# Optimization experiments

Measured on AMD Instinct MI355X. Metric: run time of the kernel, lower is better.

The kernel has to match this reference:

```python
import jax, jax.numpy as jnp
import numpy as np

N_HEAD = 16
ROPE_CACHE = 2500  # Rotary module caches tables of length 2500
NEG_INF = -1e30


def _rope_tables(head_dim):
    inv_freq = 1.0 / (10000.0 ** (jnp.arange(0, head_dim, 2, dtype=jnp.float32) / head_dim))
    t = jnp.arange(ROPE_CACHE, dtype=jnp.float32)
    freqs = t[:, None] * inv_freq[None, :]            # (2500, head_dim//2)
    emb = jnp.concatenate([freqs, freqs], axis=-1)    # (2500, head_dim)
    return jnp.cos(emb), jnp.sin(emb)


def _rotate_half(x):
    h = x.shape[-1] // 2
    return jnp.concatenate([-x[..., h:], x[..., :h]], axis=-1)


def setup_inputs() -> dict:
    key = jax.random.key(0)
    ks = jax.random.split(key, 8)
    B, S, D = 2, 2048, 1024
    H = N_HEAD
    hd = D // H
    return {
        "qx": jax.random.normal(ks[0], (B, S, D), jnp.float32),
        "kvx": jax.random.normal(ks[1], (B, S, D), jnp.float32),
        "k_cache": jnp.zeros((B, H, S, hd), jnp.float32),
        "v_cache": jnp.zeros((B, H, S, hd), jnp.float32),
        "Wq": jax.random.normal(ks[2], (D, D), jnp.float32) * 0.02,
        "bq": jnp.zeros((D,), jnp.float32),
        "Wk": jax.random.normal(ks[3], (D, D), jnp.float32) * 0.02,
        "Wv": jax.random.normal(ks[4], (D, D), jnp.float32) * 0.02,
        "bv": jnp.zeros((D,), jnp.float32),
        "Wo": jax.random.normal(ks[5], (D, D), jnp.float32) * 0.02,
        "bo": jnp.zeros((D,), jnp.float32),
        "q_positions": jnp.arange(S, dtype=jnp.int32),
        "kv_positions": jnp.arange(S, dtype=jnp.int32),
    }


def reference(qx, kvx, k_cache, v_cache, Wq, bq, Wk, Wv, bv, Wo, bo, q_positions, kv_positions):
    B, Sq, D = qx.shape
    H = N_HEAD
    hd = D // H
    Skv = kvx.shape[1]
    cos, sin = _rope_tables(hd)
    # sqrt_qk_scale = sqrt(1) = 1, folded out.

    def rope(x, pos):  # x: (B, S, H, hd)
        c = cos[pos][None, :, None, :]
        s = sin[pos][None, :, None, :]
        return x * c + _rotate_half(x) * s

    # projections (torch Linear: y = x @ W.T + b; key has no bias)
    q = (qx @ Wq.T + bq).reshape(B, Sq, H, hd)
    q = rope(q, q_positions).transpose(0, 2, 1, 3)            # (B,H,Sq,hd)
    k = (kvx @ Wk.T).reshape(B, Skv, H, hd)
    k = rope(k, kv_positions).transpose(0, 2, 1, 3)           # (B,H,Skv,hd)
    v = (kvx @ Wv.T + bv).reshape(B, Skv, H, hd).transpose(0, 2, 1, 3)

    # KV-cache scatter update: k_cache[:, :, kv_positions] = k
    k_cache = k_cache.at[:, :, kv_positions].set(k)
    v_cache = v_cache.at[:, :, kv_positions].set(v)
    Sc = k_cache.shape[2]

    # SDPA (causal), scaled by 1/sqrt(head_dim) as in F.scaled_dot_product_attention
    scores = jnp.einsum('bhqd,bhkd->bhqk', q, k_cache) / jnp.sqrt(jnp.float32(hd))
    causal = jnp.arange(Sq)[:, None] >= jnp.arange(Sc)[None, :]
    scores = jnp.where(causal[None, None], scores, NEG_INF)
    attn = jax.nn.softmax(scores, axis=-1)
    wv = jnp.einsum('bhqk,bhkd->bhqd', attn, v_cache)

    out = wv.transpose(0, 2, 1, 3).reshape(B, Sq, D) @ Wo.T + bo
    return out
```

## Files before the change

### kernel.cpp

```cpp
#include <hip/hip_runtime.h>
#include <cstdint>
#include <cstddef>

#define NH   16
#define SEQ  2048
#define DM   1024
#define HD   64
#define KDIM 1024
#define MROWS 4096
#define CH   2

using short8  = __attribute__((ext_vector_type(8))) short;
using short4v = __attribute__((ext_vector_type(4))) short;
using floatx4 = __attribute__((ext_vector_type(4))) float;

__device__ __forceinline__ short f2bf(float f) {
  unsigned int u = __float_as_uint(f);
  u += 0x7fffu + ((u >> 16) & 1u);
  return (short)(u >> 16);
}
__device__ __forceinline__ float bf2f(short s) {
  return __uint_as_float(((unsigned int)(unsigned short)s) << 16);
}
__device__ __forceinline__ unsigned int pktrunc(float lo, float hi) {
  return __builtin_amdgcn_perm(__float_as_uint(hi), __float_as_uint(lo),
                               0x07060302u);
}

__device__ __forceinline__ void async_ld16(const void* g, void* l) {
  __builtin_amdgcn_global_load_lds(
      (const __attribute__((address_space(1))) void*)g,
      (__attribute__((address_space(3))) void*)l, 16, 0, 0);
}

struct Cvt8 {
  const float* src[8];
  void* dst[8];
  int n[8];
  const int* pos[8];
};

__global__ void convert8(Cvt8 a) {
  const int which = blockIdx.y;
  const int stride = gridDim.x * blockDim.x;
  if (which < 6) {
    const float4* s = (const float4*)a.src[which];
    short4v* d = (short4v*)a.dst[which];
    const int n4 = a.n[which] >> 2;
    for (int i = blockIdx.x * blockDim.x + threadIdx.x; i < n4; i += stride) {
      float4 v = s[i];
      short4v o;
      o.x = f2bf(v.x); o.y = f2bf(v.y); o.z = f2bf(v.z); o.w = f2bf(v.w);
      d[i] = o;
    }
  } else {
    const int* pos = a.pos[which];
    float2* d = (float2*)a.dst[which];
    const int n = a.n[which];
    for (int i = blockIdx.x * blockDim.x + threadIdx.x; i < n; i += stride) {
      int s = i >> 5, d1 = i & 31;
      float fr = __powf(10000.f, -(float)d1 * (1.f / 32.f));
      float ang = (float)pos[s] * fr;
      float sn, cs;
      __sincosf(ang, &sn, &cs);
      d[i] = make_float2(cs, sn);
    }
  }
}

__device__ __forceinline__ void gemm_core(const short* __restrict__ A,
                                          const short* __restrict__ B,
                                          int row0, int col0,
                                          short* As, short* Bs,
                                          floatx4 (&acc)[4][4], int tid) {
  const int lane = tid & 63;
  const int w = tid >> 6;
  const int quad = lane >> 4;
  const int ln = lane & 15;
  const int wr = w >> 1, wc = w & 1;
  const int swz = (quad ^ ((ln >> 1) & 3)) * 8;

#pragma unroll
  for (int i = 0; i < 4; ++i)
#pragma unroll
    for (int j = 0; j < 4; ++j) acc[i][j] = (floatx4){0.f, 0.f, 0.f, 0.f};

  for (int k0 = 0; k0 < KDIM; k0 += 64) {
    __syncthreads();
#pragma unroll
    for (int g = 0; g < 4; ++g) {
      int slot = g * 256 + tid;
      int kk = slot >> 9;
      int row = (slot >> 2) & 127;
      int grp = (slot & 3) ^ ((slot >> 3) & 3);
      int src = k0 + kk * 32 + grp * 8;
      async_ld16(A + (size_t)(row0 + row) * KDIM + src, As + slot * 8);
      async_ld16(B + (size_t)(col0 + row) * KDIM + src, Bs + slot * 8);
    }
    __syncthreads();

#pragma unroll
    for (int ks = 0; ks < 2; ++ks) {
      short8 af[4], bfr[4];
#pragma unroll
      for (int i = 0; i < 4; ++i)
        af[i] = *(const short8*)(As + ks * 4096 + (wr * 64 + i * 16 + ln) * 32 + swz);
#pragma unroll
      for (int j = 0; j < 4; ++j)
        bfr[j] = *(const short8*)(Bs + ks * 4096 + (wc * 64 + j * 16 + ln) * 32 + swz);
#pragma unroll
      for (int i = 0; i < 4; ++i)
#pragma unroll
        for (int j = 0; j < 4; ++j)
          acc[i][j] = __builtin_amdgcn_mfma_f32_16x16x32_bf16(af[i], bfr[j], acc[i][j], 0, 0, 0);
    }
  }
}

__global__ __launch_bounds__(256) void proj_gemm(
    const short* __restrict__ qxb, const short* __restrict__ kvxb,
    const short* __restrict__ Wqb, const short* __restrict__ Wkb,
    const short* __restrict__ Wvb,
    const float* __restrict__ bq, const float* __restrict__ bv,
    short* __restrict__ Qo, short* __restrict__ Ko, short* __restrict__ Vt,
    const float2* __restrict__ qtab, const float2* __restrict__ ktab) {
  __shared__ __align__(16) short As[128 * 64];
  __shared__ __align__(16) short Bs[128 * 64];

  const int tid = threadIdx.x;
  const int lane = tid & 63;
  const int w = tid >> 6;
  const int quad = lane >> 4;
  const int ln = lane & 15;
  const int wr = w >> 1, wc = w & 1;
  const int z = blockIdx.z;

  int row0, col0;
  const short *A, *B;
  if (z == 2) {
    A = Wvb; B = kvxb;
    row0 = blockIdx.x * 128;
    col0 = blockIdx.y * 128;
  } else {
    A = z ? kvxb : qxb;
    B = z ? Wkb : Wqb;
    row0 = blockIdx.y * 128;
    col0 = blockIdx.x * 128;
  }

  floatx4 acc[4][4];
  gemm_core(A, B, row0, col0, As, Bs, acc, tid);

  if (z == 2) {
#pragma unroll
    for (int i = 0; i < 4; ++i)
#pragma unroll
      for (int r = 0; r < 4; ++r) {
        int nr = row0 + wr * 64 + i * 16 + quad * 4 + r;
        int h = nr >> 6, d = nr & 63;
        float bb = bv[nr];
        size_t base = ((size_t)(h)*HD + d) * SEQ;
#pragma unroll
        for (int j = 0; j < 4; ++j) {
          int sc = col0 + wc * 64 + j * 16 + ln;
          int b = sc >> 11, s = sc & (SEQ - 1);
          Vt[((size_t)b * NH * HD) * SEQ + base + s] = f2bf(acc[i][j][r] + bb);
        }
      }
  } else {
    const int colbase = col0 + wc * 64;
    const float scale = (z == 0) ? 0.125f : 1.0f;
    const float* bias = (z == 0) ? bq : nullptr;
    const float2* tab = (z == 0) ? qtab : ktab;
    short* Out = (z == 0) ? Qo : Ko;
#pragma unroll
    for (int j = 0; j < 2; ++j) {
      int col1 = colbase + j * 16 + ln;
      float b1 = bias ? bias[col1] : 0.f;
      float b2 = bias ? bias[col1 + 32] : 0.f;
      int h = col1 >> 6;
      int d1 = col1 & 63;
#pragma unroll
      for (int i = 0; i < 4; ++i)
#pragma unroll
        for (int r = 0; r < 4; ++r) {
          int row = row0 + wr * 64 + i * 16 + quad * 4 + r;
          int b = row >> 11, s = row & (SEQ - 1);
          float2 cs_sn = tab[s * 32 + d1];
          float x1 = acc[i][j][r] + b1;
          float x2 = acc[i][j + 2][r] + b2;
          float o1 = (x1 * cs_sn.x - x2 * cs_sn.y) * scale;
          float o2 = (x2 * cs_sn.x + x1 * cs_sn.y) * scale;
          size_t basq = ((((size_t)b * NH + h) * SEQ) + s) * HD;
          Out[basq + d1] = f2bf(o1);
          Out[basq + d1 + 32] = f2bf(o2);
        }
    }
  }
}

__global__ __launch_bounds__(256) void out_gemm(
    const short* __restrict__ Po, const float* __restrict__ Lo,
    const short* __restrict__ Bb,
    const float* __restrict__ bias, float* __restrict__ out) {
  __shared__ __align__(16) short As[64 * 64];
  __shared__ __align__(16) short Bs[128 * 64];
  const int tid = threadIdx.x;
  const int lane = tid & 63;
  const int w = tid >> 6;
  const int quad = lane >> 4;
  const int ln = lane & 15;
  const int wr = w >> 1, wc = w & 1;
  const int swz = (quad ^ ((ln >> 1) & 3)) * 8;
  const int row0 = (blockIdx.x >> 3) * 64;
  const int col0 = (blockIdx.x & 7) * 128;
  const int b16 = (row0 >> 11) * 16;
  const int qt = (row0 & (SEQ - 1)) >> 6;

  floatx4 acc[2][4];
#pragma unroll
  for (int i = 0; i < 2; ++i)
#pragma unroll
    for (int j = 0; j < 4; ++j) acc[i][j] = (floatx4){0.f, 0.f, 0.f, 0.f};

  for (int k0 = 0; k0 < KDIM; k0 += 64) {
    __syncthreads();
    {
      const int h = k0 >> 6;
      const size_t ib = ((size_t)(b16 + h) * 32 + qt) * CH;
      const short* P0 = Po + (ib + 0) * 4096;
      const short* P1 = Po + (ib + 1) * 4096;
      const float* L0 = Lo + (ib + 0) * 64;
      const float* L1 = Lo + (ib + 1) * 64;
#pragma unroll
      for (int g = 0; g < 2; ++g) {
        int slot = g * 256 + tid;
        int kk = slot >> 8;
        int row = (slot >> 2) & 63;
        int grp = (slot & 3) ^ ((slot >> 3) & 3);
        int off = row * 64 + kk * 32 + grp * 8;
        short8 a0 = *(const short8*)(P0 + off);
        short8 a1 = *(const short8*)(P1 + off);
        float inv = 1.f / (L0[row] + L1[row]);
        float v[8];
#pragma unroll
        for (int e = 0; e < 8; ++e) v[e] = (bf2f(a0[e]) + bf2f(a1[e])) * inv;
        uint4 u;
        u.x = pktrunc(v[0], v[1]);
        u.y = pktrunc(v[2], v[3]);
        u.z = pktrunc(v[4], v[5]);
        u.w = pktrunc(v[6], v[7]);
        *(uint4*)(As + slot * 8) = u;
      }
#pragma unroll
      for (int g = 0; g < 4; ++g) {
        int slot = g * 256 + tid;
        int kk = slot >> 9;
        int row = (slot >> 2) & 127;
        int grp = (slot & 3) ^ ((slot >> 3) & 3);
        async_ld16(Bb + (size_t)(col0 + row) * KDIM + k0 + kk * 32 + grp * 8,
                   Bs + slot * 8);
      }
    }
    __syncthreads();

#pragma unroll
    for (int ks = 0; ks < 2; ++ks) {
      short8 af[2], bfr[4];
#pragma unroll
      for (int i = 0; i < 2; ++i)
        af[i] = *(const short8*)(As + ks * 2048 + (wr * 32 + i * 16 + ln) * 32 + swz);
#pragma unroll
      for (int j = 0; j < 4; ++j)
        bfr[j] = *(const short8*)(Bs + ks * 4096 + (wc * 64 + j * 16 + ln) * 32 + swz);
#pragma unroll
      for (int i = 0; i < 2; ++i)
#pragma unroll
        for (int j = 0; j < 4; ++j)
          acc[i][j] = __builtin_amdgcn_mfma_f32_16x16x32_bf16(af[i], bfr[j], acc[i][j], 0, 0, 0);
    }
  }

#pragma unroll
  for (int j = 0; j < 4; ++j) {
    int col = col0 + wc * 64 + j * 16 + ln;
    float bb = bias[col];
#pragma unroll
    for (int i = 0; i < 2; ++i)
#pragma unroll
      for (int r = 0; r < 4; ++r) {
        int row = row0 + wr * 32 + i * 16 + quad * 4 + r;
        out[(size_t)row * DM + col] = acc[i][j][r] + bb;
      }
  }
}

__global__ __launch_bounds__(256) void attn_partial(
    const short* __restrict__ Q, const short* __restrict__ Kc,
    const short* __restrict__ Vtg, short* __restrict__ Po,
    float* __restrict__ Lo) {
  const int tid = threadIdx.x;
  const int lane = tid & 63;
  const int w = tid >> 6;
  const int quad = lane >> 4;
  const int ln = lane & 15;
  const int swz = (quad ^ ((ln >> 1) & 3)) * 8;
  const int bh = blockIdx.y;
  const int bx = blockIdx.x;
  const int qt = 31 - (bx >> 1);
  const int ch = bx & (CH - 1);
  const size_t idx = ((size_t)bh * 32 + qt) * CH + ch;

  if (ch > qt) {
    short8 z = (short8){0, 0, 0, 0, 0, 0, 0, 0};
    short8* Pz = (short8*)(Po + idx * 4096);
    Pz[tid] = z;
    Pz[256 + tid] = z;
    if (tid < 64) Lo[idx * 64 + tid] = 0.f;
    return;
  }

  const int q0 = qt * 64;
  const int wlo = q0 + w * 16;

  const short* Qb = Q + (size_t)bh * SEQ * HD;
  const short* Kb = Kc + (size_t)bh * SEQ * HD;
  const short* Vb = Vtg + (size_t)bh * HD * SEQ;

  __shared__ __align__(16) short Ks[2 * 64 * 32];
  __shared__ __align__(16) short Vs[2 * 64 * 32];
  __shared__ __align__(16) short Pt[4][16 * 72];

  short8 qa[2];
#pragma unroll
  for (int kk = 0; kk < 2; ++kk)
    qa[kk] = *(const short8*)(Qb + (size_t)(wlo + ln) * HD + quad * 8 + kk * 32);

  floatx4 oacc[4];
  float lp = 0.f;
#pragma unroll
  for (int jd = 0; jd < 4; ++jd) oacc[jd] = (floatx4){0.f, 0.f, 0.f, 0.f};

  for (int t = ch * 64; t <= q0; t += CH * 64) {
    __syncthreads();
#pragma unroll
    for (int g = 0; g < 2; ++g) {
      int slot = (w * 2 + g) * 64 + lane;
      int kk = slot >> 8;
      int rowi = (slot >> 2) & 63;
      int grp = (slot & 3) ^ ((slot >> 3) & 3);
      async_ld16(Kb + (size_t)(t + rowi) * HD + kk * 32 + grp * 8,
                 (char*)Ks + slot * 16);
      async_ld16(Vb + (size_t)rowi * SEQ + t + kk * 32 + grp * 8,
                 (char*)Vs + slot * 16);
    }
    __syncthreads();

    floatx4 sacc[4];
#pragma unroll
    for (int c = 0; c < 4; ++c) sacc[c] = (floatx4){0.f, 0.f, 0.f, 0.f};
#pragma unroll
    for (int kk = 0; kk < 2; ++kk)
#pragma unroll
      for (int c = 0; c < 4; ++c) {
        short8 kb = *(const short8*)(Ks + kk * 2048 + (c * 16 + ln) * 32 + swz);
        sacc[c] = __builtin_amdgcn_mfma_f32_16x16x32_bf16(kb, qa[kk], sacc[c], 0, 0, 0);
      }

    const bool dmask = (t == q0);
#pragma unroll
    for (int c = 0; c < 4; ++c) {
      float p[4];
#pragma unroll
      for (int r = 0; r < 4; ++r) {
        float pv = __expf(sacc[c][r]);
        if (dmask) {
          int sp = t + c * 16 + quad * 4 + r;
          int qq = wlo + ln;
          if (sp > qq) pv = 0.f;
        }
        lp += pv;
        p[r] = pv;
      }
      uint2 uu;
      uu.x = pktrunc(p[0], p[1]);
      uu.y = pktrunc(p[2], p[3]);
      *(uint2*)(&Pt[w][ln * 72 + c * 16 + quad * 4]) = uu;
    }

#pragma unroll
    for (int kk = 0; kk < 2; ++kk) {
      short8 pb = *(const short8*)(&Pt[w][ln * 72 + kk * 32 + quad * 8]);
#pragma unroll
      for (int jd = 0; jd < 4; ++jd) {
        short8 va = *(const short8*)(Vs + kk * 2048 + (jd * 16 + ln) * 32 + swz);
        oacc[jd] = __builtin_amdgcn_mfma_f32_16x16x32_bf16(va, pb, oacc[jd], 0, 0, 0);
      }
    }
  }

  short* Pob = Po + idx * 4096;
#pragma unroll
  for (int jd = 0; jd < 4; ++jd) {
    short4v pk;
#pragma unroll
    for (int r = 0; r < 4; ++r) pk[r] = f2bf(oacc[jd][r]);
    *(short4v*)(Pob + (w * 16 + ln) * 64 + jd * 16 + quad * 4) = pk;
  }
  float l = lp;
  l += __shfl_xor(l, 16, 64);
  l += __shfl_xor(l, 32, 64);
  if (quad == 0) Lo[idx * 64 + w * 16 + ln] = l;
}

extern "C" void kernel_launch(void* const* d_in, const int* in_sizes, int n_in,
                              void* d_out, int out_size, void* d_ws, size_t ws_size,
                              hipStream_t stream) {
  const float* qx  = (const float*)d_in[0];
  const float* kvx = (const float*)d_in[1];
  const float* Wq = (const float*)d_in[4];
  const float* bq = (const float*)d_in[5];
  const float* Wk = (const float*)d_in[6];
  const float* Wv = (const float*)d_in[7];
  const float* bv = (const float*)d_in[8];
  const float* Wo = (const float*)d_in[9];
  const float* bo = (const float*)d_in[10];
  const int* qpos  = (const int*)d_in[11];
  const int* kvpos = (const int*)d_in[12];

  char* ws = (char*)d_ws;
  short* qxb  = (short*)(ws + 0);
  short* kvxb = (short*)(ws + 8388608);
  short* Wqb  = (short*)(ws + 16777216);
  short* Wkb  = (short*)(ws + 18874368);
  short* Wvb  = (short*)(ws + 20971520);
  short* Wob  = (short*)(ws + 23068672);
  short* Qbf  = (short*)(ws + 25165824);
  short* Kbf  = (short*)(ws + 33554432);
  short* Vtb  = (short*)(ws + 41943040);
  float2* qtab = (float2*)(ws + 50331648);
  float2* ktab = (float2*)(ws + 50331648 + 524288);
  short* Po = (short*)(ws + 0);
  float* Lo = (float*)(ws + 16777216);

  Cvt8 c;
  c.src[0] = qx;  c.dst[0] = qxb;  c.n[0] = MROWS * KDIM; c.pos[0] = nullptr;
  c.src[1] = kvx; c.dst[1] = kvxb; c.n[1] = MROWS * KDIM; c.pos[1] = nullptr;
  c.src[2] = Wq;  c.dst[2] = Wqb;  c.n[2] = DM * KDIM;    c.pos[2] = nullptr;
  c.src[3] = Wk;  c.dst[3] = Wkb;  c.n[3] = DM * KDIM;    c.pos[3] = nullptr;
  c.src[4] = Wv;  c.dst[4] = Wvb;  c.n[4] = DM * KDIM;    c.pos[4] = nullptr;
  c.src[5] = Wo;  c.dst[5] = Wob;  c.n[5] = DM * KDIM;    c.pos[5] = nullptr;
  c.src[6] = nullptr; c.dst[6] = qtab; c.n[6] = SEQ * 32; c.pos[6] = qpos;
  c.src[7] = nullptr; c.dst[7] = ktab; c.n[7] = SEQ * 32; c.pos[7] = kvpos;
  convert8<<<dim3(1024, 8), 256, 0, stream>>>(c);

  proj_gemm<<<dim3(DM / 128, MROWS / 128, 3), 256, 0, stream>>>(
      qxb, kvxb, Wqb, Wkb, Wvb, bq, bv, Qbf, Kbf, Vtb, qtab, ktab);

  attn_partial<<<dim3(32 * CH, 2 * NH), 256, 0, stream>>>(Qbf, Kbf, Vtb, Po, Lo);

  out_gemm<<<dim3(64 * 8), 256, 0, stream>>>(Po, Lo, Wob, bo, (float*)d_out);
}
```

Baseline: 253.4 us.

## Use two waves per attention block, each handling 32 query rows

```diff
diff --git a/kernel.cpp b/kernel.cpp
--- a/kernel.cpp
+++ b/kernel.cpp
@@ -295,7 +295,7 @@
   }
 }
 
-__global__ __launch_bounds__(256) void attn_partial(
+__global__ __launch_bounds__(128) void attn_partial(
     const short* __restrict__ Q, const short* __restrict__ Kc,
     const short* __restrict__ Vtg, short* __restrict__ Po,
     float* __restrict__ Lo) {
@@ -314,14 +314,14 @@
   if (ch > qt) {
     short8 z = (short8){0, 0, 0, 0, 0, 0, 0, 0};
     short8* Pz = (short8*)(Po + idx * 4096);
-    Pz[tid] = z;
-    Pz[256 + tid] = z;
+#pragma unroll
+    for (int k = 0; k < 4; ++k) Pz[k * 128 + tid] = z;
     if (tid < 64) Lo[idx * 64 + tid] = 0.f;
     return;
   }
 
   const int q0 = qt * 64;
-  const int wlo = q0 + w * 16;
+  const int wlo = q0 + w * 32;
 
   const short* Qb = Q + (size_t)bh * SEQ * HD;
   const short* Kb = Kc + (size_t)bh * SEQ * HD;
@@ -329,23 +329,29 @@
 
   __shared__ __align__(16) short Ks[2 * 64 * 32];
   __shared__ __align__(16) short Vs[2 * 64 * 32];
-  __shared__ __align__(16) short Pt[4][16 * 72];
-
-  short8 qa[2];
-#pragma unroll
-  for (int kk = 0; kk < 2; ++kk)
-    qa[kk] = *(const short8*)(Qb + (size_t)(wlo + ln) * HD + quad * 8 + kk * 32);
-
-  floatx4 oacc[4];
-  float lp = 0.f;
-#pragma unroll
-  for (int jd = 0; jd < 4; ++jd) oacc[jd] = (floatx4){0.f, 0.f, 0.f, 0.f};
+  __shared__ __align__(16) short Pt[2][32 * 72];
+
+  short8 qa[2][2];
+#pragma unroll
+  for (int i = 0; i < 2; ++i)
+#pragma unroll
+    for (int kk = 0; kk < 2; ++kk)
+      qa[i][kk] = *(const short8*)(Qb + (size_t)(wlo + i * 16 + ln) * HD +
+                                   quad * 8 + kk * 32);
+
+  floatx4 oacc[4][2];
+  float lp[2];
+#pragma unroll
+  for (int jd = 0; jd < 4; ++jd)
+#pragma unroll
+    for (int i = 0; i < 2; ++i) oacc[jd][i] = (floatx4){0.f, 0.f, 0.f, 0.f};
+  lp[0] = lp[1] = 0.f;
 
   for (int t = ch * 64; t <= q0; t += CH * 64) {
     __syncthreads();
 #pragma unroll
-    for (int g = 0; g < 2; ++g) {
-      int slot = (w * 2 + g) * 64 + lane;
+    for (int g = 0; g < 4; ++g) {
+      int slot = (w * 4 + g) * 64 + lane;
       int kk = slot >> 8;
       int rowi = (slot >> 2) & 63;
       int grp = (slot & 3) ^ ((slot >> 3) & 3);
@@ -356,61 +362,73 @@
     }
     __syncthreads();
 
-    floatx4 sacc[4];
-#pragma unroll
-    for (int c = 0; c < 4; ++c) sacc[c] = (floatx4){0.f, 0.f, 0.f, 0.f};
+    floatx4 sacc[4][2];
+#pragma unroll
+    for (int c = 0; c < 4; ++c)
+#pragma unroll
+      for (int i = 0; i < 2; ++i) sacc[c][i] = (floatx4){0.f, 0.f, 0.f, 0.f};
 #pragma unroll
     for (int kk = 0; kk < 2; ++kk)
 #pragma unroll
       for (int c = 0; c < 4; ++c) {
         short8 kb = *(const short8*)(Ks + kk * 2048 + (c * 16 + ln) * 32 + swz);
-        sacc[c] = __builtin_amdgcn_mfma_f32_16x16x32_bf16(kb, qa[kk], sacc[c], 0, 0, 0);
-      }
-
-    const bool dmask = (t == q0);
-#pragma unroll
-    for (int c = 0; c < 4; ++c) {
-      float p[4];
-#pragma unroll
-      for (int r = 0; r < 4; ++r) {
-        float pv = __expf(sacc[c][r]);
-        if (dmask) {
-          int sp = t + c * 16 + quad * 4 + r;
-          int qq = wlo + ln;
-          if (sp > qq) pv = 0.f;
+        sacc[c][0] = __builtin_amdgcn_mfma_f32_16x16x32_bf16(kb, qa[0][kk], sacc[c][0], 0, 0, 0);
+        sacc[c][1] = __builtin_amdgcn_mfma_f32_16x16x32_bf16(kb, qa[1][kk], sacc[c][1], 0, 0, 0);
+      }
+
+    const bool dmask = (t + 63 > wlo);
+#pragma unroll
+    for (int c = 0; c < 4; ++c)
+#pragma unroll
+      for (int i = 0; i < 2; ++i) {
+        float p[4];
+#pragma unroll
+        for (int r = 0; r < 4; ++r) {
+          float pv = __expf(sacc[c][i][r]);
+          if (dmask) {
+            int sp = t + c * 16 + quad * 4 + r;
+            int qq = wlo + i * 16 + ln;
+            if (sp > qq) pv = 0.f;
+          }
+          lp[i] += pv;
+          p[r] = pv;
         }
-        lp += pv;
-        p[r] = pv;
-      }
-      uint2 uu;
-      uu.x = pktrunc(p[0], p[1]);
-      uu.y = pktrunc(p[2], p[3]);
-      *(uint2*)(&Pt[w][ln * 72 + c * 16 + quad * 4]) = uu;
-    }
+        uint2 uu;
+        uu.x = pktrunc(p[0], p[1]);
+        uu.y = pktrunc(p[2], p[3]);
+        *(uint2*)(&Pt[w][(i * 16 + ln) * 72 + c * 16 + quad * 4]) = uu;
+      }
 
 #pragma unroll
     for (int kk = 0; kk < 2; ++kk) {
-      short8 pb = *(const short8*)(&Pt[w][ln * 72 + kk * 32 + quad * 8]);
+      short8 pb0 = *(const short8*)(&Pt[w][(ln) * 72 + kk * 32 + quad * 8]);
+      short8 pb1 = *(const short8*)(&Pt[w][(16 + ln) * 72 + kk * 32 + quad * 8]);
 #pragma unroll
       for (int jd = 0; jd < 4; ++jd) {
         short8 va = *(const short8*)(Vs + kk * 2048 + (jd * 16 + ln) * 32 + swz);
-        oacc[jd] = __builtin_amdgcn_mfma_f32_16x16x32_bf16(va, pb, oacc[jd], 0, 0, 0);
+        oacc[jd][0] = __builtin_amdgcn_mfma_f32_16x16x32_bf16(va, pb0, oacc[jd][0], 0, 0, 0);
+        oacc[jd][1] = __builtin_amdgcn_mfma_f32_16x16x32_bf16(va, pb1, oacc[jd][1], 0, 0, 0);
       }
     }
   }
 
   short* Pob = Po + idx * 4096;
 #pragma unroll
-  for (int jd = 0; jd < 4; ++jd) {
-    short4v pk;
-#pragma unroll
-    for (int r = 0; r < 4; ++r) pk[r] = f2bf(oacc[jd][r]);
-    *(short4v*)(Pob + (w * 16 + ln) * 64 + jd * 16 + quad * 4) = pk;
-  }
-  float l = lp;
-  l += __shfl_xor(l, 16, 64);
-  l += __shfl_xor(l, 32, 64);
-  if (quad == 0) Lo[idx * 64 + w * 16 + ln] = l;
+  for (int jd = 0; jd < 4; ++jd)
+#pragma unroll
+    for (int i = 0; i < 2; ++i) {
+      short4v pk;
+#pragma unroll
+      for (int r = 0; r < 4; ++r) pk[r] = f2bf(oacc[jd][i][r]);
+      *(short4v*)(Pob + (w * 32 + i * 16 + ln) * 64 + jd * 16 + quad * 4) = pk;
+    }
+#pragma unroll
+  for (int i = 0; i < 2; ++i) {
+    float l = lp[i];
+    l += __shfl_xor(l, 16, 64);
+    l += __shfl_xor(l, 32, 64);
+    if (quad == 0) Lo[idx * 64 + w * 32 + i * 16 + ln] = l;
+  }
 }
 
 extern "C" void kernel_launch(void* const* d_in, const int* in_sizes, int n_in,
@@ -457,7 +475,7 @@
   proj_gemm<<<dim3(DM / 128, MROWS / 128, 3), 256, 0, stream>>>(
       qxb, kvxb, Wqb, Wkb, Wvb, bq, bv, Qbf, Kbf, Vtb, qtab, ktab);
 
-  attn_partial<<<dim3(32 * CH, 2 * NH), 256, 0, stream>>>(Qbf, Kbf, Vtb, Po, Lo);
+  attn_partial<<<dim3(32 * CH, 2 * NH), 128, 0, stream>>>(Qbf, Kbf, Vtb, Po, Lo);
 
   out_gemm<<<dim3(64 * 8), 256, 0, stream>>>(Po, Lo, Wob, bo, (float*)d_out);
 }
```

Result: no change. 253.9 us (+0.2%).
